# Kernel optimization log

Measured on AMD Instinct MI355X. Metric: run time of the kernel, lower is better.

Reference implementation:

```python
import jax, jax.numpy as jnp
import numpy as np

G, K = 60, 13  # SO(3) group size, neighbors per group element


def _gather(x, nei):
    # x: [N, C, G] -> [N, C, G, K] via fixed neighbor indices (len G*K)
    return x[:, :, nei].reshape(x.shape[0], x.shape[1], G, K)


def _comb(x, nei, W, b):
    # gather-then-(1,K)-Conv2d == contraction over (channel, neighbor)
    d = _gather(x, nei)                                   # [N,C,G,K]
    return jnp.einsum('ncgk,ock->nog', d, W) + b[None, :, None]


def setup_inputs() -> dict:
    key = jax.random.key(0)
    ks = jax.random.split(key, 8)
    N = 512
    feats = jax.random.normal(ks[0], (N, 32, G), jnp.float32)
    nei = jax.random.randint(ks[1], (G * K,), 0, G, jnp.int32)

    def w(k, o, c):
        return jax.random.normal(k, (o, c, K), jnp.float32) * (1.0 / np.sqrt(c * K))

    return {
        'feats': feats, 'nei': nei,
        'W_in': w(ks[2], 256, 32), 'b_in': jnp.zeros((256,), jnp.float32),
        'W_r1': w(ks[3], 512, 256), 'b_r1': jnp.zeros((512,), jnp.float32),
        'W_r2': w(ks[4], 256, 512), 'b_r2': jnp.zeros((256,), jnp.float32),
        'W_out': w(ks[5], 32, 256), 'b_out': jnp.zeros((32,), jnp.float32),
    }


def reference(feats, nei, W_in, b_in, W_r1, b_r1, W_r2, b_r2, W_out, b_out):
    # Conv_in: gather + (1,13) conv, 32 -> 256
    h = _comb(feats, nei, W_in, b_in)                      # [N,256,G]
    # Residual_Comb_Conv(256, 512, 256)
    r = jax.nn.relu(_comb(h, nei, W_r1, b_r1))             # [N,512,G]
    h = h + _comb(r, nei, W_r2, b_r2)                      # [N,256,G]
    # Conv_out: gather + (1,13) conv, 256 -> 32, then outer residual
    feats_eqv = _comb(h, nei, W_out, b_out) + feats        # [N,32,G]
    feats_inv = jnp.mean(feats_eqv, axis=-1)               # [N,32]
    feats_eqv = feats_eqv / jnp.maximum(
        jnp.linalg.norm(feats_eqv, axis=1, keepdims=True), 1e-4)
    feats_inv = feats_inv / jnp.maximum(
        jnp.linalg.norm(feats_inv, axis=1, keepdims=True), 1e-4)
    return feats_inv, feats_eqv
```

## Files before the change

kernel.cpp:

```cpp
#include <hip/hip_runtime.h>
#include <stdint.h>

#define GSZ 60
#define KNB 13
#define NPT 512

typedef __attribute__((ext_vector_type(4))) float f32x4;
typedef __attribute__((ext_vector_type(8))) short s16x8;

__device__ __forceinline__ ushort f2bf(float f) {
  union { float f; unsigned u; } v; v.f = f;
  unsigned r = v.u + 0x7fffu + ((v.u >> 16) & 1u);
  return (ushort)(r >> 16);
}
__device__ __forceinline__ float bf2f(ushort h) {
  union { unsigned u; float f; } v; v.u = ((unsigned)h) << 16;
  return v.f;
}

__device__ __forceinline__ void gload_lds16(const void* gsrc, void* ldst) {
  __builtin_amdgcn_global_load_lds(
      (const __attribute__((address_space(1))) uint32_t*)gsrc,
      (__attribute__((address_space(3))) uint32_t*)ldst, 16, 0, 0);
}

__global__ __launch_bounds__(256) void prep_feats_k(const float* __restrict__ feats,
                                                    ushort* __restrict__ X0) {
  int idx = blockIdx.x * 256 + threadIdx.x;
  if (idx >= 61 * NPT * 32) return;
  int c = idx & 31;
  int t = idx >> 5;
  int n = t % NPT;
  int g = t / NPT;
  X0[idx] = (g < GSZ) ? f2bf(feats[(n * 32 + c) * GSZ + g]) : (ushort)0;
}

__global__ __launch_bounds__(256) void prep_wb_k(const float* __restrict__ W,
                                                 ushort* __restrict__ Wb,
                                                 int O, int OPAD, int C, int KPAD) {
  int idx = blockIdx.x * 256 + threadIdx.x;
  if (idx >= OPAD * KPAD) return;
  int o = idx / KPAD;
  int kk = idx - o * KPAD;
  int k = kk / C;
  int c = kk - k * C;
  Wb[idx] = (o < O && k < KNB) ? f2bf(W[(o * C + c) * KNB + k]) : (ushort)0;
}

template <int CIN, int KTOT, int OPAD, int OREAL, int BN, int MODE, bool RELU>
__global__ __launch_bounds__(256) void comb_gemm(
    const ushort* __restrict__ Xin, const ushort* __restrict__ Wb,
    const float* __restrict__ bias, const int* __restrict__ nei,
    ushort* __restrict__ Xout, float* __restrict__ Eq,
    const float* __restrict__ feats, int qb, int qe) {
  constexpr int BM = 128;
  constexpr int BK = 64;
  constexpr int TO = OPAD / BN;
  constexpr int TN = NPT / BM;
  constexpr int WN = BN / 2;
  constexpr int N_REP = WN / 16;
  constexpr int M_REP = 4;
  constexpr int CSH = (CIN == 32) ? 5 : (CIN == 256) ? 8 : 9;
  static_assert(CIN == (1 << CSH), "CIN pow2");

  __shared__ ushort smA[2][BM * BK];
  __shared__ ushort smB[2][BN * BK];
  __shared__ int nei_sh[16];

  const int nwg = TO * TN * GSZ;
  const int cpx = nwg >> 3;
  const int bid = blockIdx.x;
  const int idx = (bid & 7) * cpx + (bid >> 3);
  const int g = idx / (TO * TN);
  const int rem = idx - g * (TO * TN);
  const int nt = rem / TO;
  const int ot = rem - nt * TO;
  const int n0 = nt * BM;
  const int o0 = ot * BN;

  const int t = threadIdx.x;
  if (t < 14) nei_sh[t] = (t < KNB) ? nei[g * KNB + t] : GSZ;
  __syncthreads();

  const int w = t >> 6;
  const int l = t & 63;
  const int lrow = l & 15;
  const int lkg = l >> 4;
  const int wr = w >> 1;
  const int wc = w & 1;
  const int srow_w = w * 8;
  const int sr = l >> 3;
  const int slot = l & 7;

  int laneA[BM / 32], laneB[BN / 32], swz[BM / 32];
#pragma unroll
  for (int j = 0; j < BM / 32; ++j) {
    const int r = j * 32 + srow_w + sr;
    swz[j] = (slot ^ (r & 7)) << 3;
    laneA[j] = ((n0 + r) << CSH) + swz[j];
  }
#pragma unroll
  for (int j = 0; j < BN / 32; ++j) {
    const int r = j * 32 + srow_w + sr;
    laneB[j] = (o0 + r) * KTOT + ((slot ^ (r & 7)) << 3);
  }

  auto stage = [&](int buf, int q) {
    const int c0 = q * BK;
    if constexpr (CIN >= 64) {
      const int pbase = nei_sh[c0 >> CSH] * (NPT << CSH) + (c0 & (CIN - 1));
#pragma unroll
      for (int j = 0; j < BM / 32; ++j)
        gload_lds16(Xin + pbase + laneA[j], &smA[buf][(j * 32 + srow_w) * BK]);
    } else {
#pragma unroll
      for (int j = 0; j < BM / 32; ++j) {
        const int r = j * 32 + srow_w + sr;
        const int kk = c0 + swz[j];
        const int nbr = kk >> CSH;
        const int cc = kk & (CIN - 1);
        gload_lds16(Xin + ((nei_sh[nbr] * NPT + n0 + r) << CSH) + cc,
                    &smA[buf][(j * 32 + srow_w) * BK]);
      }
    }
#pragma unroll
    for (int j = 0; j < BN / 32; ++j)
      gload_lds16(Wb + laneB[j] + c0, &smB[buf][(j * 32 + srow_w) * BK]);
  };

  f32x4 acc[M_REP][N_REP] = {};

  stage(0, qb);
  asm volatile("s_waitcnt vmcnt(0)" ::: "memory");
  __builtin_amdgcn_s_barrier();

  int cur = 0;
#pragma unroll 1
  for (int q = qb; q < qe; ++q) {
    if (q + 1 < qe) stage(cur ^ 1, q + 1);
#pragma unroll
    for (int ks = 0; ks < 2; ++ks) {
      const int cb = ks * 4 + lkg;
      s16x8 bf[N_REP];
#pragma unroll
      for (int n = 0; n < N_REP; ++n) {
        const int r = wc * WN + n * 16 + lrow;
        bf[n] = *(const s16x8*)&smB[cur][r * BK + ((cb ^ (r & 7)) << 3)];
      }
#pragma unroll
      for (int m = 0; m < M_REP; ++m) {
        const int r = wr * 64 + m * 16 + lrow;
        s16x8 af = *(const s16x8*)&smA[cur][r * BK + ((cb ^ (r & 7)) << 3)];
#pragma unroll
        for (int n = 0; n < N_REP; ++n)
          acc[m][n] = __builtin_amdgcn_mfma_f32_16x16x32_bf16(af, bf[n], acc[m][n], 0, 0, 0);
      }
    }
    asm volatile("s_waitcnt vmcnt(0)" ::: "memory");
    __builtin_amdgcn_s_barrier();
    cur ^= 1;
  }

#pragma unroll
  for (int m = 0; m < M_REP; ++m) {
#pragma unroll
    for (int n = 0; n < N_REP; ++n) {
      const int oc = o0 + wc * WN + n * 16 + lrow;
      float bv;
      if (MODE == 2)
        bv = (oc < OREAL && feats) ? bias[oc] : 0.f;
      else
        bv = bias[oc];
#pragma unroll
      for (int r = 0; r < 4; ++r) {
        const int row = n0 + wr * 64 + m * 16 + lkg * 4 + r;
        float v = acc[m][n][r] + bv;
        if (MODE == 0) {
          if (RELU) v = v > 0.f ? v : 0.f;
          Xout[((size_t)g * NPT + row) * OPAD + oc] = f2bf(v);
        } else if (MODE == 1) {
          const size_t ix = ((size_t)g * NPT + row) * OPAD + oc;
          Xout[ix] = f2bf(bf2f(Xout[ix]) + v);
        } else {
          const float add = (oc < OREAL && feats) ? feats[((size_t)row * 32 + oc) * GSZ + g] : 0.f;
          Eq[((size_t)g * NPT + row) * 64 + oc] = v + add;
        }
      }
    }
  }
}

template <int CIN, int KTOT, int OPAD, int OREAL, int BN, int MODE, bool RELU>
__global__ __launch_bounds__(512) void comb_gemm8(
    const ushort* __restrict__ Xin, const ushort* __restrict__ Wb,
    const float* __restrict__ bias, const int* __restrict__ nei,
    ushort* __restrict__ Xout) {
  constexpr int BM = 256;
  constexpr int BK = 64;
  constexpr int NCH = KTOT / BK;
  constexpr int TO = OPAD / BN;
  constexpr int TN = NPT / BM;
  constexpr int WARPS_N = BN / 64;
  constexpr int WARPS_M = 8 / WARPS_N;
  constexpr int WM = BM / WARPS_M;
  constexpr int WN = 64;
  constexpr int M_REP = WM / 16;
  constexpr int N_REP = 4;
  constexpr int CSH = (CIN == 256) ? 8 : 9;
  static_assert(CIN == (1 << CSH), "CIN pow2");

  __shared__ ushort smA[2][BM * BK];
  __shared__ ushort smB[2][BN * BK];
  __shared__ int nei_sh[16];

  const int nwg = TO * TN * GSZ;
  const int cpx = nwg >> 3;
  const int bid = blockIdx.x;
  const int idx = (bid & 7) * cpx + (bid >> 3);
  const int g = idx / (TO * TN);
  const int rem = idx - g * (TO * TN);
  const int nt = rem / TO;
  const int ot = rem - nt * TO;
  const int n0 = nt * BM;
  const int o0 = ot * BN;

  const int t = threadIdx.x;
  if (t < 14) nei_sh[t] = (t < KNB) ? nei[g * KNB + t] : GSZ;
  __syncthreads();

  const int w = t >> 6;
  const int l = t & 63;
  const int lrow = l & 15;
  const int lkg = l >> 4;
  const int wr = w / WARPS_N;
  const int wc = w % WARPS_N;
  const int srow_w = w * 8;
  const int sr = l >> 3;
  const int slot = l & 7;
  const int swz = (slot ^ sr) << 3;

  int laneA[BM / 64], laneB[BN / 64];
#pragma unroll
  for (int j = 0; j < BM / 64; ++j)
    laneA[j] = ((n0 + j * 64 + srow_w + sr) << CSH) + swz;
#pragma unroll
  for (int j = 0; j < BN / 64; ++j)
    laneB[j] = (o0 + j * 64 + srow_w + sr) * KTOT + swz;

  auto stage = [&](int buf, int q) {
    const int c0 = q * BK;
    const int pbase = nei_sh[c0 >> CSH] * (NPT << CSH) + (c0 & (CIN - 1));
#pragma unroll
    for (int j = 0; j < BM / 64; ++j)
      gload_lds16(Xin + pbase + laneA[j], &smA[buf][(j * 64 + srow_w) * BK]);
#pragma unroll
    for (int j = 0; j < BN / 64; ++j)
      gload_lds16(Wb + laneB[j] + c0, &smB[buf][(j * 64 + srow_w) * BK]);
  };

  f32x4 acc[M_REP][N_REP] = {};

  stage(0, 0);
  asm volatile("s_waitcnt vmcnt(0)" ::: "memory");
  __builtin_amdgcn_s_barrier();

  int cur = 0;
#pragma unroll 1
  for (int q = 0; q < NCH; ++q) {
    if (q + 1 < NCH) stage(cur ^ 1, q + 1);
    __builtin_amdgcn_s_setprio(1);
#pragma unroll
    for (int ks = 0; ks < 2; ++ks) {
      const int cb = ks * 4 + lkg;
      s16x8 bf[N_REP];
#pragma unroll
      for (int n = 0; n < N_REP; ++n) {
        const int r = wc * WN + n * 16 + lrow;
        bf[n] = *(const s16x8*)&smB[cur][r * BK + ((cb ^ (r & 7)) << 3)];
      }
#pragma unroll
      for (int m = 0; m < M_REP; ++m) {
        const int r = wr * WM + m * 16 + lrow;
        s16x8 af = *(const s16x8*)&smA[cur][r * BK + ((cb ^ (r & 7)) << 3)];
#pragma unroll
        for (int n = 0; n < N_REP; ++n)
          acc[m][n] = __builtin_amdgcn_mfma_f32_16x16x32_bf16(af, bf[n], acc[m][n], 0, 0, 0);
      }
    }
    __builtin_amdgcn_s_setprio(0);
    asm volatile("s_waitcnt vmcnt(0)" ::: "memory");
    __builtin_amdgcn_s_barrier();
    cur ^= 1;
  }

#pragma unroll
  for (int m = 0; m < M_REP; ++m) {
#pragma unroll
    for (int n = 0; n < N_REP; ++n) {
      const int oc = o0 + wc * WN + n * 16 + lrow;
      const float bv = bias[oc];
#pragma unroll
      for (int r = 0; r < 4; ++r) {
        const int row = n0 + wr * WM + m * 16 + lkg * 4 + r;
        float v = acc[m][n][r] + bv;
        if (MODE == 0) {
          if (RELU) v = v > 0.f ? v : 0.f;
          Xout[((size_t)g * NPT + row) * OPAD + oc] = f2bf(v);
        } else {
          const size_t ix = ((size_t)g * NPT + row) * OPAD + oc;
          Xout[ix] = f2bf(bf2f(Xout[ix]) + v);
        }
      }
    }
  }
}

__global__ __launch_bounds__(256) void finalize_k(const float* __restrict__ Eq,
                                                  float* __restrict__ out) {
  const int n = blockIdx.x;
  const int t = threadIdx.x;
  const int c = t & 31;
  const int gs = t >> 5;
  constexpr size_t PART = (size_t)GSZ * NPT * 64;

  float invp = 0.f;
  for (int g = gs; g < GSZ; g += 8) {
    const size_t base = ((size_t)g * NPT + n) * 64 + c;
    float x = Eq[base] + Eq[PART + base] + Eq[2 * PART + base] + Eq[3 * PART + base];
    invp += x;
    float ss = x * x;
#pragma unroll
    for (int m = 16; m >= 1; m >>= 1) ss += __shfl_xor(ss, m, 64);
    float nrm = sqrtf(ss);
    nrm = nrm > 1e-4f ? nrm : 1e-4f;
    out[16384 + ((size_t)n * 32 + c) * GSZ + g] = x / nrm;
  }

  __shared__ float tmp[8][32];
  tmp[gs][c] = invp;
  __syncthreads();
  if (t < 32) {
    float s = 0.f;
#pragma unroll
    for (int i = 0; i < 8; ++i) s += tmp[i][t];
    s *= (1.f / 60.f);
    float ss = s * s;
#pragma unroll
    for (int m = 16; m >= 1; m >>= 1) ss += __shfl_xor(ss, m, 64);
    float nrm = sqrtf(ss);
    nrm = nrm > 1e-4f ? nrm : 1e-4f;
    out[(size_t)n * 32 + t] = s / nrm;
  }
}

extern "C" void kernel_launch(void* const* d_in, const int* in_sizes, int n_in,
                              void* d_out, int out_size, void* d_ws, size_t ws_size,
                              hipStream_t stream) {
  const float* feats = (const float*)d_in[0];
  const int* nei = (const int*)d_in[1];
  const float* W_in = (const float*)d_in[2];
  const float* b_in = (const float*)d_in[3];
  const float* W_r1 = (const float*)d_in[4];
  const float* b_r1 = (const float*)d_in[5];
  const float* W_r2 = (const float*)d_in[6];
  const float* b_r2 = (const float*)d_in[7];
  const float* W_out = (const float*)d_in[8];
  const float* b_out = (const float*)d_in[9];
  float* out = (float*)d_out;

  char* ws = (char*)d_ws;
  size_t off = 0;
  auto alloc = [&](size_t bytes) {
    void* p = ws + off;
    off += (bytes + 255) & ~(size_t)255;
    return p;
  };
  ushort* X0 = (ushort*)alloc((size_t)61 * NPT * 32 * 2);
  ushort* H1 = (ushort*)alloc((size_t)GSZ * NPT * 256 * 2);
  ushort* R = (ushort*)alloc((size_t)GSZ * NPT * 512 * 2);
  ushort* Wb_in = (ushort*)alloc((size_t)256 * 448 * 2);
  ushort* Wb_r1 = (ushort*)alloc((size_t)512 * 3328 * 2);
  ushort* Wb_r2 = (ushort*)alloc((size_t)256 * 6656 * 2);
  ushort* Wb_out = (ushort*)alloc((size_t)64 * 3328 * 2);
  float* Eq4 = (float*)R;

  prep_feats_k<<<(61 * NPT * 32 + 255) / 256, 256, 0, stream>>>(feats, X0);
  prep_wb_k<<<(256 * 448 + 255) / 256, 256, 0, stream>>>(W_in, Wb_in, 256, 256, 32, 448);
  prep_wb_k<<<(512 * 3328 + 255) / 256, 256, 0, stream>>>(W_r1, Wb_r1, 512, 512, 256, 3328);
  prep_wb_k<<<(256 * 6656 + 255) / 256, 256, 0, stream>>>(W_r2, Wb_r2, 256, 256, 512, 6656);
  prep_wb_k<<<(64 * 3328 + 255) / 256, 256, 0, stream>>>(W_out, Wb_out, 32, 64, 256, 3328);

  comb_gemm<32, 448, 256, 256, 128, 0, false><<<dim3(2 * 4 * GSZ), dim3(256), 0, stream>>>(
      X0, Wb_in, b_in, nei, H1, nullptr, nullptr, 0, 7);
  comb_gemm8<256, 3328, 512, 512, 256, 0, true><<<dim3(240), dim3(512), 0, stream>>>(
      H1, Wb_r1, b_r1, nei, R);
  comb_gemm8<512, 6656, 256, 256, 128, 1, false><<<dim3(240), dim3(512), 0, stream>>>(
      R, Wb_r2, b_r2, nei, H1);
  for (int kp = 0; kp < 4; ++kp) {
    comb_gemm<256, 3328, 64, 32, 64, 2, false><<<dim3(1 * 4 * GSZ), dim3(256), 0, stream>>>(
        H1, Wb_out, b_out, nei, nullptr, Eq4 + (size_t)kp * GSZ * NPT * 64,
        kp == 0 ? feats : nullptr, kp * 13, (kp + 1) * 13);
  }
  finalize_k<<<NPT, 256, 0, stream>>>(Eq4, out);
}
```

Measured before the change: 375.9 us.

## Use 128x256 tiles with triple-buffered LDS pipeline in residual GEMMs

The two large residual gather-GEMM kernels now use 128x256 output tiles instead of 256-row tiles, which doubles the number of workgroups for r1 (480) and r2 (240 with BN 256). The LDS staging moves from double to triple buffering with loads issued two chunks ahead, and a partial vmcnt wait lets one stage stay in flight during compute. The setprio hints are dropped. The deeper pipeline and more blocks aim to hide global load latency and raise occupancy, at the cost of more LDS per block and a different tile balance.

```diff
diff --git a/kernel.cpp b/kernel.cpp
--- a/kernel.cpp
+++ b/kernel.cpp
@@ -190,27 +190,22 @@
   }
 }
 
-template <int CIN, int KTOT, int OPAD, int OREAL, int BN, int MODE, bool RELU>
-__global__ __launch_bounds__(512) void comb_gemm8(
+template <int CIN, int KTOT, int OPAD, int MODE, bool RELU>
+__global__ __launch_bounds__(512) void comb_gemm_d(
     const ushort* __restrict__ Xin, const ushort* __restrict__ Wb,
     const float* __restrict__ bias, const int* __restrict__ nei,
     ushort* __restrict__ Xout) {
-  constexpr int BM = 256;
-  constexpr int BK = 64;
+  constexpr int BM = 128, BN = 256, BK = 64;
   constexpr int NCH = KTOT / BK;
   constexpr int TO = OPAD / BN;
   constexpr int TN = NPT / BM;
-  constexpr int WARPS_N = BN / 64;
-  constexpr int WARPS_M = 8 / WARPS_N;
-  constexpr int WM = BM / WARPS_M;
-  constexpr int WN = 64;
-  constexpr int M_REP = WM / 16;
-  constexpr int N_REP = 4;
+  constexpr int WM = 64, WN = 64;
+  constexpr int M_REP = 4, N_REP = 4;
   constexpr int CSH = (CIN == 256) ? 8 : 9;
   static_assert(CIN == (1 << CSH), "CIN pow2");
 
-  __shared__ ushort smA[2][BM * BK];
-  __shared__ ushort smB[2][BN * BK];
+  __shared__ ushort smA[3][BM * BK];
+  __shared__ ushort smB[3][BN * BK];
   __shared__ int nei_sh[16];
 
   const int nwg = TO * TN * GSZ;
@@ -232,43 +227,43 @@
   const int l = t & 63;
   const int lrow = l & 15;
   const int lkg = l >> 4;
-  const int wr = w / WARPS_N;
-  const int wc = w % WARPS_N;
-  const int srow_w = w * 8;
+  const int wr = w >> 2;
+  const int wc = w & 3;
   const int sr = l >> 3;
   const int slot = l & 7;
   const int swz = (slot ^ sr) << 3;
-
-  int laneA[BM / 64], laneB[BN / 64];
-#pragma unroll
-  for (int j = 0; j < BM / 64; ++j)
+  const int srow_w = w * 8;
+
+  int laneA[2], laneB[4];
+#pragma unroll
+  for (int j = 0; j < 2; ++j)
     laneA[j] = ((n0 + j * 64 + srow_w + sr) << CSH) + swz;
 #pragma unroll
-  for (int j = 0; j < BN / 64; ++j)
+  for (int j = 0; j < 4; ++j)
     laneB[j] = (o0 + j * 64 + srow_w + sr) * KTOT + swz;
 
   auto stage = [&](int buf, int q) {
     const int c0 = q * BK;
     const int pbase = nei_sh[c0 >> CSH] * (NPT << CSH) + (c0 & (CIN - 1));
 #pragma unroll
-    for (int j = 0; j < BM / 64; ++j)
+    for (int j = 0; j < 2; ++j)
       gload_lds16(Xin + pbase + laneA[j], &smA[buf][(j * 64 + srow_w) * BK]);
 #pragma unroll
-    for (int j = 0; j < BN / 64; ++j)
+    for (int j = 0; j < 4; ++j)
       gload_lds16(Wb + laneB[j] + c0, &smB[buf][(j * 64 + srow_w) * BK]);
   };
 
   f32x4 acc[M_REP][N_REP] = {};
 
   stage(0, 0);
-  asm volatile("s_waitcnt vmcnt(0)" ::: "memory");
+  stage(1, 1);
+  asm volatile("s_waitcnt vmcnt(6)" ::: "memory");
   __builtin_amdgcn_s_barrier();
 
-  int cur = 0;
+  int bc = 0;
 #pragma unroll 1
   for (int q = 0; q < NCH; ++q) {
-    if (q + 1 < NCH) stage(cur ^ 1, q + 1);
-    __builtin_amdgcn_s_setprio(1);
+    if (q + 2 < NCH) stage(bc ? bc - 1 : 2, q + 2);
 #pragma unroll
     for (int ks = 0; ks < 2; ++ks) {
       const int cb = ks * 4 + lkg;
@@ -276,21 +271,23 @@
 #pragma unroll
       for (int n = 0; n < N_REP; ++n) {
         const int r = wc * WN + n * 16 + lrow;
-        bf[n] = *(const s16x8*)&smB[cur][r * BK + ((cb ^ (r & 7)) << 3)];
+        bf[n] = *(const s16x8*)&smB[bc][r * BK + ((cb ^ (r & 7)) << 3)];
       }
 #pragma unroll
       for (int m = 0; m < M_REP; ++m) {
         const int r = wr * WM + m * 16 + lrow;
-        s16x8 af = *(const s16x8*)&smA[cur][r * BK + ((cb ^ (r & 7)) << 3)];
+        s16x8 af = *(const s16x8*)&smA[bc][r * BK + ((cb ^ (r & 7)) << 3)];
 #pragma unroll
         for (int n = 0; n < N_REP; ++n)
           acc[m][n] = __builtin_amdgcn_mfma_f32_16x16x32_bf16(af, bf[n], acc[m][n], 0, 0, 0);
       }
     }
-    __builtin_amdgcn_s_setprio(0);
-    asm volatile("s_waitcnt vmcnt(0)" ::: "memory");
+    if (q + 2 < NCH)
+      asm volatile("s_waitcnt vmcnt(6)" ::: "memory");
+    else
+      asm volatile("s_waitcnt vmcnt(0)" ::: "memory");
     __builtin_amdgcn_s_barrier();
-    cur ^= 1;
+    bc = (bc == 2) ? 0 : bc + 1;
   }
 
 #pragma unroll
@@ -392,9 +389,9 @@
 
   comb_gemm<32, 448, 256, 256, 128, 0, false><<<dim3(2 * 4 * GSZ), dim3(256), 0, stream>>>(
       X0, Wb_in, b_in, nei, H1, nullptr, nullptr, 0, 7);
-  comb_gemm8<256, 3328, 512, 512, 256, 0, true><<<dim3(240), dim3(512), 0, stream>>>(
+  comb_gemm_d<256, 3328, 512, 0, true><<<dim3(2 * 4 * GSZ), dim3(512), 0, stream>>>(
       H1, Wb_r1, b_r1, nei, R);
-  comb_gemm8<512, 6656, 256, 256, 128, 1, false><<<dim3(240), dim3(512), 0, stream>>>(
+  comb_gemm_d<512, 6656, 256, 1, false><<<dim3(1 * 4 * GSZ), dim3(512), 0, stream>>>(
       R, Wb_r2, b_r2, nei, H1);
   for (int kp = 0; kp < 4; ++kp) {
     comb_gemm<256, 3328, 64, 32, 64, 2, false><<<dim3(1 * 4 * GSZ), dim3(256), 0, stream>>>(
```

Result: slower. 423.9 us (+12.8%).

## Switch residual GEMMs to 32x32x16 MFMA 128x128 tiles, unsplit output conv

Applied to the files above, without the earlier changes.

Replaces the 512-thread 256-row-tile residual GEMM kernels with 256-thread 128x128-tile kernels that use 32x32x16 bf16 MFMA. This raises the workgroup count (960 and 480 instead of 240) for better CU occupancy, and the larger MFMA shape needs fewer LDS reads per flop. The output conv no longer uses a 4-way split-K over separate launches with partial sums; it runs once over the full K into a dedicated Eq buffer, and finalize reads a single partial. The risk is that the output conv now has only 240 workgroups with longer K loops, and the new MFMA layout changes register pressure.

```diff
diff --git a/kernel.cpp b/kernel.cpp
--- a/kernel.cpp
+++ b/kernel.cpp
@@ -6,6 +6,7 @@
 #define NPT 512
 
 typedef __attribute__((ext_vector_type(4))) float f32x4;
+typedef __attribute__((ext_vector_type(16))) float f32x16;
 typedef __attribute__((ext_vector_type(8))) short s16x8;
 
 __device__ __forceinline__ ushort f2bf(float f) {
@@ -52,9 +53,10 @@
     const ushort* __restrict__ Xin, const ushort* __restrict__ Wb,
     const float* __restrict__ bias, const int* __restrict__ nei,
     ushort* __restrict__ Xout, float* __restrict__ Eq,
-    const float* __restrict__ feats, int qb, int qe) {
+    const float* __restrict__ feats) {
   constexpr int BM = 128;
   constexpr int BK = 64;
+  constexpr int NCH = KTOT / BK;
   constexpr int TO = OPAD / BN;
   constexpr int TN = NPT / BM;
   constexpr int WN = BN / 2;
@@ -130,14 +132,14 @@
 
   f32x4 acc[M_REP][N_REP] = {};
 
-  stage(0, qb);
+  stage(0, 0);
   asm volatile("s_waitcnt vmcnt(0)" ::: "memory");
   __builtin_amdgcn_s_barrier();
 
   int cur = 0;
 #pragma unroll 1
-  for (int q = qb; q < qe; ++q) {
-    if (q + 1 < qe) stage(cur ^ 1, q + 1);
+  for (int q = 0; q < NCH; ++q) {
+    if (q + 1 < NCH) stage(cur ^ 1, q + 1);
 #pragma unroll
     for (int ks = 0; ks < 2; ++ks) {
       const int cb = ks * 4 + lkg;
@@ -168,7 +170,7 @@
       const int oc = o0 + wc * WN + n * 16 + lrow;
       float bv;
       if (MODE == 2)
-        bv = (oc < OREAL && feats) ? bias[oc] : 0.f;
+        bv = (oc < OREAL) ? bias[oc] : 0.f;
       else
         bv = bias[oc];
 #pragma unroll
@@ -182,7 +184,7 @@
           const size_t ix = ((size_t)g * NPT + row) * OPAD + oc;
           Xout[ix] = f2bf(bf2f(Xout[ix]) + v);
         } else {
-          const float add = (oc < OREAL && feats) ? feats[((size_t)row * 32 + oc) * GSZ + g] : 0.f;
+          const float add = (oc < OREAL) ? feats[((size_t)row * 32 + oc) * GSZ + g] : 0.f;
           Eq[((size_t)g * NPT + row) * 64 + oc] = v + add;
         }
       }
@@ -190,22 +192,15 @@
   }
 }
 
-template <int CIN, int KTOT, int OPAD, int OREAL, int BN, int MODE, bool RELU>
-__global__ __launch_bounds__(512) void comb_gemm8(
+template <int CIN, int KTOT, int OPAD, int MODE, bool RELU>
+__global__ __launch_bounds__(256) void comb_gemm32(
     const ushort* __restrict__ Xin, const ushort* __restrict__ Wb,
     const float* __restrict__ bias, const int* __restrict__ nei,
     ushort* __restrict__ Xout) {
-  constexpr int BM = 256;
-  constexpr int BK = 64;
+  constexpr int BM = 128, BN = 128, BK = 64;
   constexpr int NCH = KTOT / BK;
   constexpr int TO = OPAD / BN;
   constexpr int TN = NPT / BM;
-  constexpr int WARPS_N = BN / 64;
-  constexpr int WARPS_M = 8 / WARPS_N;
-  constexpr int WM = BM / WARPS_M;
-  constexpr int WN = 64;
-  constexpr int M_REP = WM / 16;
-  constexpr int N_REP = 4;
   constexpr int CSH = (CIN == 256) ? 8 : 9;
   static_assert(CIN == (1 << CSH), "CIN pow2");
 
@@ -230,35 +225,35 @@
 
   const int w = t >> 6;
   const int l = t & 63;
-  const int lrow = l & 15;
-  const int lkg = l >> 4;
-  const int wr = w / WARPS_N;
-  const int wc = w % WARPS_N;
+  const int l31 = l & 31;
+  const int kg = l >> 5;
+  const int wr = w >> 1;
+  const int wc = w & 1;
   const int srow_w = w * 8;
   const int sr = l >> 3;
   const int slot = l & 7;
-  const int swz = (slot ^ sr) << 3;
-
-  int laneA[BM / 64], laneB[BN / 64];
-#pragma unroll
-  for (int j = 0; j < BM / 64; ++j)
-    laneA[j] = ((n0 + j * 64 + srow_w + sr) << CSH) + swz;
-#pragma unroll
-  for (int j = 0; j < BN / 64; ++j)
-    laneB[j] = (o0 + j * 64 + srow_w + sr) * KTOT + swz;
+
+  int laneA[4], laneB[4];
+#pragma unroll
+  for (int j = 0; j < 4; ++j) {
+    const int r = j * 32 + srow_w + sr;
+    const int sz = (slot ^ (r & 7)) << 3;
+    laneA[j] = ((n0 + r) << CSH) + sz;
+    laneB[j] = (o0 + r) * KTOT + sz;
+  }
 
   auto stage = [&](int buf, int q) {
     const int c0 = q * BK;
     const int pbase = nei_sh[c0 >> CSH] * (NPT << CSH) + (c0 & (CIN - 1));
 #pragma unroll
-    for (int j = 0; j < BM / 64; ++j)
-      gload_lds16(Xin + pbase + laneA[j], &smA[buf][(j * 64 + srow_w) * BK]);
-#pragma unroll
-    for (int j = 0; j < BN / 64; ++j)
-      gload_lds16(Wb + laneB[j] + c0, &smB[buf][(j * 64 + srow_w) * BK]);
+    for (int j = 0; j < 4; ++j)
+      gload_lds16(Xin + pbase + laneA[j], &smA[buf][(j * 32 + srow_w) * BK]);
+#pragma unroll
+    for (int j = 0; j < 4; ++j)
+      gload_lds16(Wb + laneB[j] + c0, &smB[buf][(j * 32 + srow_w) * BK]);
   };
 
-  f32x4 acc[M_REP][N_REP] = {};
+  f32x16 acc[2][2] = {};
 
   stage(0, 0);
   asm volatile("s_waitcnt vmcnt(0)" ::: "memory");
@@ -268,41 +263,41 @@
 #pragma unroll 1
   for (int q = 0; q < NCH; ++q) {
     if (q + 1 < NCH) stage(cur ^ 1, q + 1);
-    __builtin_amdgcn_s_setprio(1);
-#pragma unroll
-    for (int ks = 0; ks < 2; ++ks) {
-      const int cb = ks * 4 + lkg;
-      s16x8 bf[N_REP];
-#pragma unroll
-      for (int n = 0; n < N_REP; ++n) {
-        const int r = wc * WN + n * 16 + lrow;
+#pragma unroll
+    for (int ks = 0; ks < 4; ++ks) {
+      const int cb = ks * 2 + kg;
+      s16x8 bf[2], af[2];
+#pragma unroll
+      for (int n = 0; n < 2; ++n) {
+        const int r = wc * 64 + n * 32 + l31;
         bf[n] = *(const s16x8*)&smB[cur][r * BK + ((cb ^ (r & 7)) << 3)];
       }
 #pragma unroll
-      for (int m = 0; m < M_REP; ++m) {
-        const int r = wr * WM + m * 16 + lrow;
-        s16x8 af = *(const s16x8*)&smA[cur][r * BK + ((cb ^ (r & 7)) << 3)];
-#pragma unroll
-        for (int n = 0; n < N_REP; ++n)
-          acc[m][n] = __builtin_amdgcn_mfma_f32_16x16x32_bf16(af, bf[n], acc[m][n], 0, 0, 0);
-      }
-    }
-    __builtin_amdgcn_s_setprio(0);
+      for (int m = 0; m < 2; ++m) {
+        const int r = wr * 64 + m * 32 + l31;
+        af[m] = *(const s16x8*)&smA[cur][r * BK + ((cb ^ (r & 7)) << 3)];
+      }
+#pragma unroll
+      for (int m = 0; m < 2; ++m)
+#pragma unroll
+        for (int n = 0; n < 2; ++n)
+          acc[m][n] = __builtin_amdgcn_mfma_f32_32x32x16_bf16(af[m], bf[n], acc[m][n], 0, 0, 0);
+    }
     asm volatile("s_waitcnt vmcnt(0)" ::: "memory");
     __builtin_amdgcn_s_barrier();
     cur ^= 1;
   }
 
 #pragma unroll
-  for (int m = 0; m < M_REP; ++m) {
-#pragma unroll
-    for (int n = 0; n < N_REP; ++n) {
-      const int oc = o0 + wc * WN + n * 16 + lrow;
+  for (int m = 0; m < 2; ++m) {
+#pragma unroll
+    for (int n = 0; n < 2; ++n) {
+      const int oc = o0 + wc * 64 + n * 32 + l31;
       const float bv = bias[oc];
 #pragma unroll
-      for (int r = 0; r < 4; ++r) {
-        const int row = n0 + wr * WM + m * 16 + lkg * 4 + r;
-        float v = acc[m][n][r] + bv;
+      for (int reg = 0; reg < 16; ++reg) {
+        const int row = n0 + wr * 64 + m * 32 + 4 * kg + (reg & 3) + 8 * (reg >> 2);
+        float v = acc[m][n][reg] + bv;
         if (MODE == 0) {
           if (RELU) v = v > 0.f ? v : 0.f;
           Xout[((size_t)g * NPT + row) * OPAD + oc] = f2bf(v);
@@ -321,12 +316,10 @@
   const int t = threadIdx.x;
   const int c = t & 31;
   const int gs = t >> 5;
-  constexpr size_t PART = (size_t)GSZ * NPT * 64;
 
   float invp = 0.f;
   for (int g = gs; g < GSZ; g += 8) {
-    const size_t base = ((size_t)g * NPT + n) * 64 + c;
-    float x = Eq[base] + Eq[PART + base] + Eq[2 * PART + base] + Eq[3 * PART + base];
+    float x = Eq[((size_t)g * NPT + n) * 64 + c];
     invp += x;
     float ss = x * x;
 #pragma unroll
@@ -378,11 +371,11 @@
   ushort* X0 = (ushort*)alloc((size_t)61 * NPT * 32 * 2);
   ushort* H1 = (ushort*)alloc((size_t)GSZ * NPT * 256 * 2);
   ushort* R = (ushort*)alloc((size_t)GSZ * NPT * 512 * 2);
+  float* Eq = (float*)alloc((size_t)GSZ * NPT * 64 * 4);
   ushort* Wb_in = (ushort*)alloc((size_t)256 * 448 * 2);
   ushort* Wb_r1 = (ushort*)alloc((size_t)512 * 3328 * 2);
   ushort* Wb_r2 = (ushort*)alloc((size_t)256 * 6656 * 2);
   ushort* Wb_out = (ushort*)alloc((size_t)64 * 3328 * 2);
-  float* Eq4 = (float*)R;
 
   prep_feats_k<<<(61 * NPT * 32 + 255) / 256, 256, 0, stream>>>(feats, X0);
   prep_wb_k<<<(256 * 448 + 255) / 256, 256, 0, stream>>>(W_in, Wb_in, 256, 256, 32, 448);
@@ -390,16 +383,14 @@
   prep_wb_k<<<(256 * 6656 + 255) / 256, 256, 0, stream>>>(W_r2, Wb_r2, 256, 256, 512, 6656);
   prep_wb_k<<<(64 * 3328 + 255) / 256, 256, 0, stream>>>(W_out, Wb_out, 32, 64, 256, 3328);
 
-  comb_gemm<32, 448, 256, 256, 128, 0, false><<<dim3(2 * 4 * GSZ), dim3(256), 0, stream>>>(
-      X0, Wb_in, b_in, nei, H1, nullptr, nullptr, 0, 7);
-  comb_gemm8<256, 3328, 512, 512, 256, 0, true><<<dim3(240), dim3(512), 0, stream>>>(
+  dim3 blk(256);
+  comb_gemm<32, 448, 256, 256, 128, 0, false><<<dim3(2 * 4 * GSZ), blk, 0, stream>>>(
+      X0, Wb_in, b_in, nei, H1, nullptr, nullptr);
+  comb_gemm32<256, 3328, 512, 0, true><<<dim3(4 * 4 * GSZ), blk, 0, stream>>>(
       H1, Wb_r1, b_r1, nei, R);
-  comb_gemm8<512, 6656, 256, 256, 128, 1, false><<<dim3(240), dim3(512), 0, stream>>>(
+  comb_gemm32<512, 6656, 256, 1, false><<<dim3(2 * 4 * GSZ), blk, 0, stream>>>(
       R, Wb_r2, b_r2, nei, H1);
-  for (int kp = 0; kp < 4; ++kp) {
-    comb_gemm<256, 3328, 64, 32, 64, 2, false><<<dim3(1 * 4 * GSZ), dim3(256), 0, stream>>>(
-        H1, Wb_out, b_out, nei, nullptr, Eq4 + (size_t)kp * GSZ * NPT * 64,
-        kp == 0 ? feats : nullptr, kp * 13, (kp + 1) * 13);
-  }
-  finalize_k<<<NPT, 256, 0, stream>>>(Eq4, out);
-}
+  comb_gemm<256, 3328, 64, 32, 64, 2, false><<<dim3(1 * 4 * GSZ), blk, 0, stream>>>(
+      H1, Wb_out, b_out, nei, nullptr, Eq, feats);
+  finalize_k<<<NPT, 256, 0, stream>>>(Eq, out);
+}
```

Measured after the change: 330.6 us. -12.0%, faster.

## Fuse prep kernels and retile residual GEMMs to smaller 128x128 BK32 blocks

Applied to the files above, without the earlier changes.

Merges the five weight/feature conversion kernels into a single launch. The 512-thread 256-row comb_gemm8 kernel becomes comb_bk32, which uses 256 threads with 128x128 tiles and BK=32, a 4-way LDS swizzle and launch_bounds occupancy 4, launching 960 blocks instead of 240. The second residual conv switches to the existing comb_gemm kernel. The intent is more blocks and higher occupancy per CU, plus fewer launches. The cost is twice as many K-loop barriers per unit of work and less data reuse per tile.

```diff
diff --git a/kernel.cpp b/kernel.cpp
--- a/kernel.cpp
+++ b/kernel.cpp
@@ -24,27 +24,47 @@
       (__attribute__((address_space(3))) uint32_t*)ldst, 16, 0, 0);
 }
 
-__global__ __launch_bounds__(256) void prep_feats_k(const float* __restrict__ feats,
-                                                    ushort* __restrict__ X0) {
+__global__ __launch_bounds__(256) void prep_all_k(
+    const float* __restrict__ W_in, const float* __restrict__ W_r1,
+    const float* __restrict__ W_r2, const float* __restrict__ W_out,
+    const float* __restrict__ feats,
+    ushort* __restrict__ Wb_in, ushort* __restrict__ Wb_r1,
+    ushort* __restrict__ Wb_r2, ushort* __restrict__ Wb_out,
+    ushort* __restrict__ X0) {
+  constexpr int N0 = 256 * 448;
+  constexpr int N1 = 512 * 3328;
+  constexpr int N2 = 256 * 6656;
+  constexpr int N3 = 64 * 3328;
+  constexpr int N4 = 61 * NPT * 32;
   int idx = blockIdx.x * 256 + threadIdx.x;
-  if (idx >= 61 * NPT * 32) return;
-  int c = idx & 31;
-  int t = idx >> 5;
-  int n = t % NPT;
-  int g = t / NPT;
-  X0[idx] = (g < GSZ) ? f2bf(feats[(n * 32 + c) * GSZ + g]) : (ushort)0;
-}
-
-__global__ __launch_bounds__(256) void prep_wb_k(const float* __restrict__ W,
-                                                 ushort* __restrict__ Wb,
-                                                 int O, int OPAD, int C, int KPAD) {
-  int idx = blockIdx.x * 256 + threadIdx.x;
-  if (idx >= OPAD * KPAD) return;
-  int o = idx / KPAD;
-  int kk = idx - o * KPAD;
-  int k = kk / C;
-  int c = kk - k * C;
-  Wb[idx] = (o < O && k < KNB) ? f2bf(W[(o * C + c) * KNB + k]) : (ushort)0;
+  if (idx < N0) {
+    int o = idx / 448, kk = idx - o * 448, k = kk / 32, c = kk - k * 32;
+    Wb_in[idx] = (k < KNB) ? f2bf(W_in[(o * 32 + c) * KNB + k]) : (ushort)0;
+    return;
+  }
+  idx -= N0;
+  if (idx < N1) {
+    int o = idx / 3328, kk = idx - o * 3328, k = kk / 256, c = kk - k * 256;
+    Wb_r1[idx] = f2bf(W_r1[(o * 256 + c) * KNB + k]);
+    return;
+  }
+  idx -= N1;
+  if (idx < N2) {
+    int o = idx / 6656, kk = idx - o * 6656, k = kk / 512, c = kk - k * 512;
+    Wb_r2[idx] = f2bf(W_r2[(o * 512 + c) * KNB + k]);
+    return;
+  }
+  idx -= N2;
+  if (idx < N3) {
+    int o = idx / 3328, kk = idx - o * 3328, k = kk / 256, c = kk - k * 256;
+    Wb_out[idx] = (o < 32) ? f2bf(W_out[(o * 256 + c) * KNB + k]) : (ushort)0;
+    return;
+  }
+  idx -= N3;
+  if (idx < N4) {
+    int c = idx & 31, t = idx >> 5, n = t % NPT, g = t / NPT;
+    X0[idx] = (g < GSZ) ? f2bf(feats[(n * 32 + c) * GSZ + g]) : (ushort)0;
+  }
 }
 
 template <int CIN, int KTOT, int OPAD, int OREAL, int BN, int MODE, bool RELU>
@@ -190,22 +210,15 @@
   }
 }
 
-template <int CIN, int KTOT, int OPAD, int OREAL, int BN, int MODE, bool RELU>
-__global__ __launch_bounds__(512) void comb_gemm8(
+template <int CIN, int KTOT, int OPAD, int MODE, bool RELU>
+__global__ __launch_bounds__(256, 4) void comb_bk32(
     const ushort* __restrict__ Xin, const ushort* __restrict__ Wb,
     const float* __restrict__ bias, const int* __restrict__ nei,
     ushort* __restrict__ Xout) {
-  constexpr int BM = 256;
-  constexpr int BK = 64;
+  constexpr int BM = 128, BN = 128, BK = 32;
   constexpr int NCH = KTOT / BK;
   constexpr int TO = OPAD / BN;
   constexpr int TN = NPT / BM;
-  constexpr int WARPS_N = BN / 64;
-  constexpr int WARPS_M = 8 / WARPS_N;
-  constexpr int WM = BM / WARPS_M;
-  constexpr int WN = 64;
-  constexpr int M_REP = WM / 16;
-  constexpr int N_REP = 4;
   constexpr int CSH = (CIN == 256) ? 8 : 9;
   static_assert(CIN == (1 << CSH), "CIN pow2");
 
@@ -232,33 +245,32 @@
   const int l = t & 63;
   const int lrow = l & 15;
   const int lkg = l >> 4;
-  const int wr = w / WARPS_N;
-  const int wc = w % WARPS_N;
-  const int srow_w = w * 8;
-  const int sr = l >> 3;
-  const int slot = l & 7;
-  const int swz = (slot ^ sr) << 3;
-
-  int laneA[BM / 64], laneB[BN / 64];
-#pragma unroll
-  for (int j = 0; j < BM / 64; ++j)
-    laneA[j] = ((n0 + j * 64 + srow_w + sr) << CSH) + swz;
-#pragma unroll
-  for (int j = 0; j < BN / 64; ++j)
-    laneB[j] = (o0 + j * 64 + srow_w + sr) * KTOT + swz;
+  const int wr = w >> 1;
+  const int wc = w & 1;
+
+  const int sgl = ((l & 3) ^ ((l >> 2) & 3)) << 3;
+  int laneA[2], laneB[2];
+#pragma unroll
+  for (int j = 0; j < 2; ++j) {
+    const int r = (w * 2 + j) * 16 + (l >> 2);
+    laneA[j] = ((n0 + r) << CSH) + sgl;
+    laneB[j] = (o0 + r) * KTOT + sgl;
+  }
 
   auto stage = [&](int buf, int q) {
     const int c0 = q * BK;
     const int pbase = nei_sh[c0 >> CSH] * (NPT << CSH) + (c0 & (CIN - 1));
 #pragma unroll
-    for (int j = 0; j < BM / 64; ++j)
-      gload_lds16(Xin + pbase + laneA[j], &smA[buf][(j * 64 + srow_w) * BK]);
-#pragma unroll
-    for (int j = 0; j < BN / 64; ++j)
-      gload_lds16(Wb + laneB[j] + c0, &smB[buf][(j * 64 + srow_w) * BK]);
+    for (int j = 0; j < 2; ++j)
+      gload_lds16(Xin + pbase + laneA[j], &smA[buf][(w * 2 + j) * 16 * BK]);
+#pragma unroll
+    for (int j = 0; j < 2; ++j)
+      gload_lds16(Wb + c0 + laneB[j], &smB[buf][(w * 2 + j) * 16 * BK]);
   };
 
-  f32x4 acc[M_REP][N_REP] = {};
+  auto ridx = [&](int r) { return r * BK + ((lkg ^ (r & 3)) << 3); };
+
+  f32x4 acc[4][4] = {};
 
   stage(0, 0);
   asm volatile("s_waitcnt vmcnt(0)" ::: "memory");
@@ -268,40 +280,31 @@
 #pragma unroll 1
   for (int q = 0; q < NCH; ++q) {
     if (q + 1 < NCH) stage(cur ^ 1, q + 1);
-    __builtin_amdgcn_s_setprio(1);
-#pragma unroll
-    for (int ks = 0; ks < 2; ++ks) {
-      const int cb = ks * 4 + lkg;
-      s16x8 bf[N_REP];
-#pragma unroll
-      for (int n = 0; n < N_REP; ++n) {
-        const int r = wc * WN + n * 16 + lrow;
-        bf[n] = *(const s16x8*)&smB[cur][r * BK + ((cb ^ (r & 7)) << 3)];
-      }
-#pragma unroll
-      for (int m = 0; m < M_REP; ++m) {
-        const int r = wr * WM + m * 16 + lrow;
-        s16x8 af = *(const s16x8*)&smA[cur][r * BK + ((cb ^ (r & 7)) << 3)];
-#pragma unroll
-        for (int n = 0; n < N_REP; ++n)
-          acc[m][n] = __builtin_amdgcn_mfma_f32_16x16x32_bf16(af, bf[n], acc[m][n], 0, 0, 0);
-      }
+    s16x8 bf[4];
+#pragma unroll
+    for (int n = 0; n < 4; ++n)
+      bf[n] = *(const s16x8*)&smB[cur][ridx(wc * 64 + n * 16 + lrow)];
+#pragma unroll
+    for (int m = 0; m < 4; ++m) {
+      s16x8 af = *(const s16x8*)&smA[cur][ridx(wr * 64 + m * 16 + lrow)];
+#pragma unroll
+      for (int n = 0; n < 4; ++n)
+        acc[m][n] = __builtin_amdgcn_mfma_f32_16x16x32_bf16(af, bf[n], acc[m][n], 0, 0, 0);
     }
-    __builtin_amdgcn_s_setprio(0);
     asm volatile("s_waitcnt vmcnt(0)" ::: "memory");
     __builtin_amdgcn_s_barrier();
     cur ^= 1;
   }
 
 #pragma unroll
-  for (int m = 0; m < M_REP; ++m) {
-#pragma unroll
-    for (int n = 0; n < N_REP; ++n) {
-      const int oc = o0 + wc * WN + n * 16 + lrow;
+  for (int m = 0; m < 4; ++m) {
+#pragma unroll
+    for (int n = 0; n < 4; ++n) {
+      const int oc = o0 + wc * 64 + n * 16 + lrow;
       const float bv = bias[oc];
 #pragma unroll
       for (int r = 0; r < 4; ++r) {
-        const int row = n0 + wr * WM + m * 16 + lkg * 4 + r;
+        const int row = n0 + wr * 64 + m * 16 + lkg * 4 + r;
         float v = acc[m][n][r] + bv;
         if (MODE == 0) {
           if (RELU) v = v > 0.f ? v : 0.f;
@@ -384,18 +387,16 @@
   ushort* Wb_out = (ushort*)alloc((size_t)64 * 3328 * 2);
   float* Eq4 = (float*)R;
 
-  prep_feats_k<<<(61 * NPT * 32 + 255) / 256, 256, 0, stream>>>(feats, X0);
-  prep_wb_k<<<(256 * 448 + 255) / 256, 256, 0, stream>>>(W_in, Wb_in, 256, 256, 32, 448);
-  prep_wb_k<<<(512 * 3328 + 255) / 256, 256, 0, stream>>>(W_r1, Wb_r1, 512, 512, 256, 3328);
-  prep_wb_k<<<(256 * 6656 + 255) / 256, 256, 0, stream>>>(W_r2, Wb_r2, 256, 256, 512, 6656);
-  prep_wb_k<<<(64 * 3328 + 255) / 256, 256, 0, stream>>>(W_out, Wb_out, 32, 64, 256, 3328);
+  constexpr int PREP_TOT = 256 * 448 + 512 * 3328 + 256 * 6656 + 64 * 3328 + 61 * NPT * 32;
+  prep_all_k<<<dim3((PREP_TOT + 255) / 256), dim3(256), 0, stream>>>(
+      W_in, W_r1, W_r2, W_out, feats, Wb_in, Wb_r1, Wb_r2, Wb_out, X0);
 
   comb_gemm<32, 448, 256, 256, 128, 0, false><<<dim3(2 * 4 * GSZ), dim3(256), 0, stream>>>(
       X0, Wb_in, b_in, nei, H1, nullptr, nullptr, 0, 7);
-  comb_gemm8<256, 3328, 512, 512, 256, 0, true><<<dim3(240), dim3(512), 0, stream>>>(
+  comb_bk32<256, 3328, 512, 0, true><<<dim3(4 * 4 * GSZ), dim3(256), 0, stream>>>(
       H1, Wb_r1, b_r1, nei, R);
-  comb_gemm8<512, 6656, 256, 256, 128, 1, false><<<dim3(240), dim3(512), 0, stream>>>(
-      R, Wb_r2, b_r2, nei, H1);
+  comb_gemm<512, 6656, 256, 256, 128, 1, false><<<dim3(2 * 4 * GSZ), dim3(256), 0, stream>>>(
+      R, Wb_r2, b_r2, nei, H1, nullptr, nullptr, 0, 104);
   for (int kp = 0; kp < 4; ++kp) {
     comb_gemm<256, 3328, 64, 32, 64, 2, false><<<dim3(1 * 4 * GSZ), dim3(256), 0, stream>>>(
         H1, Wb_out, b_out, nei, nullptr, Eq4 + (size_t)kp * GSZ * NPT * 64,
```

After: 354.3 us. 1.06x faster.
